# Kernel tuning notes

Measured on AMD Instinct MI355X. Metric: run time of the kernel, lower is better.

## Reference

```python
import jax, jax.numpy as jnp
import numpy as np

GROUPS = 32
EPS = 1e-5


def setup_inputs() -> dict:
    key = jax.random.key(0)
    k1, k2, k3, k4, k5 = jax.random.split(key, 5)
    B, C, H, W = 16, 256, 80, 80
    cg = C // GROUPS  # 8 channels per group
    x = jax.random.normal(k1, (B, C, H, W), dtype=jnp.float32)
    # conv1x1: Conv2d(cg, cg, 1) -> weight [cg, cg], bias [cg]
    fan_in = cg
    bound = 1.0 / np.sqrt(fan_in)
    conv_w = jax.random.uniform(k2, (cg, cg), minval=-bound, maxval=bound, dtype=jnp.float32)
    conv_b = jax.random.uniform(k3, (cg,), minval=-bound, maxval=bound, dtype=jnp.float32)
    # GroupNorm(num_groups=cg, num_channels=cg) affine params (init: ones/zeros)
    gn_w = jnp.ones((cg,), dtype=jnp.float32)
    gn_b = jnp.zeros((cg,), dtype=jnp.float32)
    return {"x": x, "conv_w": conv_w, "conv_b": conv_b, "gn_w": gn_w, "gn_b": gn_b}


def reference(x, conv_w, conv_b, gn_w, gn_b):
    b, c, h, w = x.shape
    cg = c // GROUPS
    gx = x.reshape(b * GROUPS, cg, h, w)  # [bg, cg, h, w]

    def norm(t):
        # GroupNorm with num_groups == num_channels: per-channel norm over (h, w)
        mu = jnp.mean(t, axis=(2, 3), keepdims=True)
        var = jnp.var(t, axis=(2, 3), keepdims=True)
        tn = (t - mu) * jax.lax.rsqrt(var + EPS)
        return tn * gn_w[None, :, None, None] + gn_b[None, :, None, None]

    def gate_branch(ph, pw):
        # ph: [bg, cg, h] (pooled over w), pw: [bg, cg, w] (pooled over h)
        cat = jnp.concatenate([ph, pw], axis=2)  # [bg, cg, h+w]
        hw = jnp.einsum('bcl,oc->bol', cat, conv_w) + conv_b[None, :, None]
        gh, gw = hw[:, :, :h], hw[:, :, h:]
        gated = gx * jax.nn.sigmoid(gh)[..., None] * jax.nn.sigmoid(gw)[:, :, None, :]
        return norm(gated)

    # avg-pool branch
    x1 = gate_branch(jnp.mean(gx, axis=3), jnp.mean(gx, axis=2))
    # max-pool branch
    y1 = gate_branch(jnp.max(gx, axis=3), jnp.max(gx, axis=2))

    x11 = x1.reshape(b * GROUPS, cg, h * w)
    y11 = y1.reshape(b * GROUPS, cg, h * w)
    # channel-attention vectors: softmax over the cg channel axis
    x12 = jax.nn.softmax(jnp.mean(x1, axis=(2, 3)), axis=-1)  # [bg, cg]  (avg pool)
    y12 = jax.nn.softmax(jnp.max(y1, axis=(2, 3)), axis=-1)   # [bg, cg]  (max pool)

    weights = jnp.einsum('bc,bcl->bl', x12, y11) + jnp.einsum('bc,bcl->bl', y12, x11)
    weights = weights.reshape(b * GROUPS, 1, h, w)
    return (gx * jax.nn.sigmoid(weights)).reshape(b, c, h, w)
```

## Files before the change

kernel.cpp:

```cpp
#include <hip/hip_runtime.h>
#include <math.h>

constexpr int CG   = 8;
constexpr int Hh   = 80;
constexpr int Ww   = 80;
constexpr int HW   = Hh * Ww;
constexpr int NG   = 16 * 32;
constexpr int NCH  = NG * CG;
constexpr int PP   = NCH * Hh;
constexpr float EPSf = 1e-5f;

constexpr int STATS = 4 * PP;

__device__ __forceinline__ float sigmoidf(float v) {
    return 1.0f / (1.0f + __expf(-v));
}

__global__ __launch_bounds__(256) void k_pool(const float* __restrict__ x,
                                              float* __restrict__ ws) {
    const int bgc = blockIdx.x;
    const float* base = x + (size_t)bgc * HW;
    __shared__ float tile[Hh * 84];

    for (int v = threadIdx.x; v < 1600; v += 256) {
        int h  = v / 20;
        int w0 = (v % 20) * 4;
        float4 d = ((const float4*)base)[v];
        *(float4*)&tile[h * 84 + w0] = d;
    }
    __syncthreads();

    const int t = threadIdx.x;
    if (t < 80) {
        float s = 0.f, m = -INFINITY;
        const float4* r = (const float4*)&tile[t * 84];
        #pragma unroll
        for (int i = 0; i < 20; i++) {
            float4 d = r[i];
            s += d.x + d.y + d.z + d.w;
            m = fmaxf(m, fmaxf(fmaxf(d.x, d.y), fmaxf(d.z, d.w)));
        }
        ws[0 * PP + bgc * 80 + t] = s * (1.f / 80.f);
        ws[2 * PP + bgc * 80 + t] = m;
    } else if (t >= 128 && t < 208) {
        const int c = t - 128;
        float s2 = 0.f, m2 = -INFINITY;
        #pragma unroll 8
        for (int i = 0; i < 80; i++) {
            float v = tile[i * 84 + c];
            s2 += v;
            m2 = fmaxf(m2, v);
        }
        ws[1 * PP + bgc * 80 + c] = s2 * (1.f / 80.f);
        ws[3 * PP + bgc * 80 + c] = m2;
    }
}

__global__ __launch_bounds__(256) void k_stats(const float* __restrict__ x,
                                               const float* __restrict__ conv_w,
                                               const float* __restrict__ conv_b,
                                               float* __restrict__ ws) {
    const int bgc = blockIdx.x;
    const int bg = bgc >> 3, o = bgc & 7;
    __shared__ float wsm[64];
    __shared__ float cbs[8];
    __shared__ float g[4 * 80];
    if (threadIdx.x < 64) wsm[threadIdx.x] = conv_w[threadIdx.x];
    if (threadIdx.x < 8)  cbs[threadIdx.x] = conv_b[threadIdx.x];
    __syncthreads();

    for (int i = threadIdx.x; i < 320; i += 256) {
        const int a = i / 80, p = i % 80;
        const float* pool = ws + a * PP + bg * 640;
        float acc = cbs[o];
        #pragma unroll
        for (int c = 0; c < 8; c++) acc += wsm[o * 8 + c] * pool[c * 80 + p];
        g[i] = sigmoidf(acc);
    }
    __syncthreads();

    const float* base = x + (size_t)bgc * HW;
    float s1x = 0.f, s2x = 0.f, s1y = 0.f, s2y = 0.f;
    float my = -INFINITY, ny = INFINITY;

    for (int i = 0; i < 7; i++) {
        const int v = threadIdx.x + i * 256;
        if (v < 1600) {
            const int h  = v / 20;
            const int w0 = (v % 20) * 4;
            float4 d = ((const float4*)base)[v];
            const float ghx = g[h], ghy = g[160 + h];
            float dd[4] = {d.x, d.y, d.z, d.w};
            #pragma unroll
            for (int j = 0; j < 4; j++) {
                const float tx = dd[j] * ghx * g[80 + w0 + j];
                const float ty = dd[j] * ghy * g[240 + w0 + j];
                s1x += tx; s2x += tx * tx;
                s1y += ty; s2y += ty * ty;
                my = fmaxf(my, ty); ny = fminf(ny, ty);
            }
        }
    }
    #pragma unroll
    for (int off = 32; off > 0; off >>= 1) {
        s1x += __shfl_down(s1x, off);
        s2x += __shfl_down(s2x, off);
        s1y += __shfl_down(s1y, off);
        s2y += __shfl_down(s2y, off);
        my = fmaxf(my, __shfl_down(my, off));
        ny = fminf(ny, __shfl_down(ny, off));
    }
    __shared__ float red[4][6];
    const int wave = threadIdx.x >> 6, lane = threadIdx.x & 63;
    if (lane == 0) {
        red[wave][0] = s1x; red[wave][1] = s2x; red[wave][2] = s1y;
        red[wave][3] = s2y; red[wave][4] = my;  red[wave][5] = ny;
    }
    __syncthreads();
    if (threadIdx.x == 0) {
        float a0 = red[0][0], a1 = red[0][1], a2 = red[0][2], a3 = red[0][3];
        float a4 = red[0][4], a5 = red[0][5];
        for (int wv = 1; wv < 4; wv++) {
            a0 += red[wv][0]; a1 += red[wv][1]; a2 += red[wv][2]; a3 += red[wv][3];
            a4 = fmaxf(a4, red[wv][4]); a5 = fminf(a5, red[wv][5]);
        }
        float* st = ws + STATS + bgc * 8;
        st[0] = a0; st[1] = a1; st[2] = a2; st[3] = a3; st[4] = a4; st[5] = a5;
    }
}

__global__ __launch_bounds__(256) void k_out(const float* __restrict__ x,
                                             const float* __restrict__ conv_w,
                                             const float* __restrict__ conv_b,
                                             const float* __restrict__ gnw,
                                             const float* __restrict__ gnb,
                                             const float* __restrict__ ws,
                                             float* __restrict__ out) {
    const int bg = blockIdx.x;
    __shared__ float wsm[64];
    __shared__ float cbs[8];
    __shared__ float g[4 * 640];
    __shared__ float Axs[8], Bxs[8], Ays[8], Bys[8], ymaxs[8];
    __shared__ float cHx[8], cHy[8];
    __shared__ float kcs;
    if (threadIdx.x < 64) wsm[threadIdx.x] = conv_w[threadIdx.x];
    if (threadIdx.x < 8)  cbs[threadIdx.x] = conv_b[threadIdx.x];
    __syncthreads();

    for (int i = threadIdx.x; i < 2560; i += 256) {
        const int a = i / 640, c = (i % 640) / 80, p = i % 80;
        const float* pool = ws + a * PP + bg * 640;
        float acc = cbs[c];
        #pragma unroll
        for (int cc = 0; cc < 8; cc++) acc += wsm[c * 8 + cc] * pool[cc * 80 + p];
        g[i] = sigmoidf(acc);
    }
    if (threadIdx.x < 8) {
        const int t = threadIdx.x;
        const float* st = ws + STATS + (bg * 8 + t) * 8;
        const float s1x = st[0], s2x = st[1], s1y = st[2], s2y = st[3];
        const float my = st[4], ny = st[5];
        const float w = gnw[t], b = gnb[t];
        const float mux  = s1x * (1.f / 6400.f);
        const float varx = s2x * (1.f / 6400.f) - mux * mux;
        const float ax   = rsqrtf(varx + EPSf) * w;
        Axs[t] = ax; Bxs[t] = b - mux * ax;
        const float muy  = s1y * (1.f / 6400.f);
        const float vary = s2y * (1.f / 6400.f) - muy * muy;
        const float ay   = rsqrtf(vary + EPSf) * w;
        Ays[t] = ay; Bys[t] = b - muy * ay;
        ymaxs[t] = (ay >= 0.f ? my : ny) * ay + Bys[t];
    }
    __syncthreads();
    if (threadIdx.x == 0) {
        float x12[8], y12[8];
        float mb = -INFINITY;
        for (int c = 0; c < 8; c++) mb = fmaxf(mb, gnb[c]);
        float se = 0.f;
        for (int c = 0; c < 8; c++) { x12[c] = __expf(gnb[c] - mb); se += x12[c]; }
        float inv = 1.f / se;
        for (int c = 0; c < 8; c++) x12[c] *= inv;
        float m2 = -INFINITY;
        for (int c = 0; c < 8; c++) m2 = fmaxf(m2, ymaxs[c]);
        se = 0.f;
        for (int c = 0; c < 8; c++) { y12[c] = __expf(ymaxs[c] - m2); se += y12[c]; }
        inv = 1.f / se;
        float kc = 0.f;
        for (int c = 0; c < 8; c++) {
            y12[c] *= inv;
            cHx[c] = y12[c] * Axs[c];
            cHy[c] = x12[c] * Ays[c];
            kc += x12[c] * Bys[c] + y12[c] * Bxs[c];
        }
        kcs = kc;
    }
    __syncthreads();
    for (int i = threadIdx.x; i < 1280; i += 256) {
        if (i < 640) g[i]        *= cHx[i / 80];
        else         g[640 + i]  *= cHy[(i - 640) / 80];
    }
    __syncthreads();

    const float kc = kcs;
    const float* base = x + (size_t)bg * CG * HW;
    float*       ob   = out + (size_t)bg * CG * HW;

    for (int i = 0; i < 7; i++) {
        const int v = threadIdx.x + i * 256;
        if (v < 1600) {
            const int h  = v / 20;
            const int w0 = (v % 20) * 4;
            float4 gxv[8];
            #pragma unroll
            for (int c = 0; c < 8; c++)
                gxv[c] = *(const float4*)(base + c * HW + v * 4);

            float s0 = kc, s1 = kc, s2 = kc, s3 = kc;
            #pragma unroll
            for (int c = 0; c < 8; c++) {
                const float chx = g[c * 80 + h];
                const float chy = g[1280 + c * 80 + h];
                const float* cwx = &g[640  + c * 80 + w0];
                const float* cwy = &g[1920 + c * 80 + w0];
                s0 += gxv[c].x * (chy * cwy[0] + chx * cwx[0]);
                s1 += gxv[c].y * (chy * cwy[1] + chx * cwx[1]);
                s2 += gxv[c].z * (chy * cwy[2] + chx * cwx[2]);
                s3 += gxv[c].w * (chy * cwy[3] + chx * cwx[3]);
            }
            s0 = sigmoidf(s0); s1 = sigmoidf(s1); s2 = sigmoidf(s2); s3 = sigmoidf(s3);
            #pragma unroll
            for (int c = 0; c < 8; c++) {
                float4 o;
                o.x = gxv[c].x * s0; o.y = gxv[c].y * s1;
                o.z = gxv[c].z * s2; o.w = gxv[c].w * s3;
                *(float4*)(ob + c * HW + v * 4) = o;
            }
        }
    }
}

extern "C" void kernel_launch(void* const* d_in, const int* in_sizes, int n_in,
                              void* d_out, int out_size, void* d_ws, size_t ws_size,
                              hipStream_t stream) {
    const float* x      = (const float*)d_in[0];
    const float* conv_w = (const float*)d_in[1];
    const float* conv_b = (const float*)d_in[2];
    const float* gn_w   = (const float*)d_in[3];
    const float* gn_b   = (const float*)d_in[4];
    float* out = (float*)d_out;
    float* ws  = (float*)d_ws;

    k_pool <<<NCH, 256, 0, stream>>>(x, ws);
    k_stats<<<NCH, 256, 0, stream>>>(x, conv_w, conv_b, ws);
    k_out  <<<NG,  256, 0, stream>>>(x, conv_w, conv_b, gn_w, gn_b, ws, out);
}
```

Baseline: 84.40 us.

## Fuse pooling, stats, and output kernels into one per-group kernel

Replaces the three-kernel pipeline (pool, per-channel stats, output) with a single kernel where each 512-thread block handles one group's 8 channels. Pooled values and GroupNorm statistics stay in shared memory instead of going through a global workspace, and the launches are reduced to one. The group's input is still read three times, relying on cache reuse, and the grid drops to 512 blocks with several serialised phases and barriers, which can reduce latency hiding.

Result: faster. 69.80 us (-17.3%).

```diff
diff --git a/kernel.cpp b/kernel.cpp
--- a/kernel.cpp
+++ b/kernel.cpp
@@ -1,192 +1,171 @@
 #include <hip/hip_runtime.h>
 #include <math.h>
 
-constexpr int CG   = 8;
-constexpr int Hh   = 80;
-constexpr int Ww   = 80;
-constexpr int HW   = Hh * Ww;
-constexpr int NG   = 16 * 32;
-constexpr int NCH  = NG * CG;
-constexpr int PP   = NCH * Hh;
+constexpr int CG = 8;
+constexpr int HW = 6400;
+constexpr int NG = 512;
 constexpr float EPSf = 1e-5f;
-
-constexpr int STATS = 4 * PP;
 
 __device__ __forceinline__ float sigmoidf(float v) {
     return 1.0f / (1.0f + __expf(-v));
 }
 
-__global__ __launch_bounds__(256) void k_pool(const float* __restrict__ x,
-                                              float* __restrict__ ws) {
-    const int bgc = blockIdx.x;
-    const float* base = x + (size_t)bgc * HW;
-    __shared__ float tile[Hh * 84];
-
-    for (int v = threadIdx.x; v < 1600; v += 256) {
-        int h  = v / 20;
-        int w0 = (v % 20) * 4;
-        float4 d = ((const float4*)base)[v];
-        *(float4*)&tile[h * 84 + w0] = d;
-    }
-    __syncthreads();
-
-    const int t = threadIdx.x;
-    if (t < 80) {
-        float s = 0.f, m = -INFINITY;
-        const float4* r = (const float4*)&tile[t * 84];
-        #pragma unroll
-        for (int i = 0; i < 20; i++) {
-            float4 d = r[i];
-            s += d.x + d.y + d.z + d.w;
-            m = fmaxf(m, fmaxf(fmaxf(d.x, d.y), fmaxf(d.z, d.w)));
-        }
-        ws[0 * PP + bgc * 80 + t] = s * (1.f / 80.f);
-        ws[2 * PP + bgc * 80 + t] = m;
-    } else if (t >= 128 && t < 208) {
-        const int c = t - 128;
-        float s2 = 0.f, m2 = -INFINITY;
-        #pragma unroll 8
-        for (int i = 0; i < 80; i++) {
-            float v = tile[i * 84 + c];
-            s2 += v;
-            m2 = fmaxf(m2, v);
-        }
-        ws[1 * PP + bgc * 80 + c] = s2 * (1.f / 80.f);
-        ws[3 * PP + bgc * 80 + c] = m2;
-    }
-}
-
-__global__ __launch_bounds__(256) void k_stats(const float* __restrict__ x,
-                                               const float* __restrict__ conv_w,
-                                               const float* __restrict__ conv_b,
-                                               float* __restrict__ ws) {
-    const int bgc = blockIdx.x;
-    const int bg = bgc >> 3, o = bgc & 7;
+__global__ __launch_bounds__(512, 4) void k_fused(
+    const float* __restrict__ x,
+    const float* __restrict__ conv_w,
+    const float* __restrict__ conv_b,
+    const float* __restrict__ gnw,
+    const float* __restrict__ gnb,
+    float* __restrict__ out)
+{
+    const int bg  = blockIdx.x;
+    const int tid = threadIdx.x;
+
+    __shared__ float tile[80 * 84];
+    __shared__ float pools[4 * 640];
+    __shared__ float g[4 * 640];
     __shared__ float wsm[64];
     __shared__ float cbs[8];
-    __shared__ float g[4 * 80];
-    if (threadIdx.x < 64) wsm[threadIdx.x] = conv_w[threadIdx.x];
-    if (threadIdx.x < 8)  cbs[threadIdx.x] = conv_b[threadIdx.x];
-    __syncthreads();
-
-    for (int i = threadIdx.x; i < 320; i += 256) {
-        const int a = i / 80, p = i % 80;
-        const float* pool = ws + a * PP + bg * 640;
-        float acc = cbs[o];
-        #pragma unroll
-        for (int c = 0; c < 8; c++) acc += wsm[o * 8 + c] * pool[c * 80 + p];
-        g[i] = sigmoidf(acc);
-    }
-    __syncthreads();
-
-    const float* base = x + (size_t)bgc * HW;
-    float s1x = 0.f, s2x = 0.f, s1y = 0.f, s2y = 0.f;
-    float my = -INFINITY, ny = INFINITY;
-
-    for (int i = 0; i < 7; i++) {
-        const int v = threadIdx.x + i * 256;
-        if (v < 1600) {
-            const int h  = v / 20;
-            const int w0 = (v % 20) * 4;
-            float4 d = ((const float4*)base)[v];
-            const float ghx = g[h], ghy = g[160 + h];
-            float dd[4] = {d.x, d.y, d.z, d.w};
-            #pragma unroll
-            for (int j = 0; j < 4; j++) {
-                const float tx = dd[j] * ghx * g[80 + w0 + j];
-                const float ty = dd[j] * ghy * g[240 + w0 + j];
+    __shared__ float stats[8][8];
+    __shared__ float Axs[8], Bxs[8], Ays[8], Bys[8], ymaxs[8], cHx[8], cHy[8];
+    __shared__ float kcs;
+
+    if (tid < 64) wsm[tid] = conv_w[tid];
+    if (tid < 8)  cbs[tid] = conv_b[tid];
+
+    const float* base = x + (size_t)bg * CG * HW;
+
+    for (int c = 0; c < 8; ++c) {
+        __syncthreads();
+        for (int i = 0; i < 4; ++i) {
+            const int v = tid + i * 512;
+            if (v < 1600) {
+                float4 d = ((const float4*)(base + c * HW))[v];
+                const int h = v / 20, w0 = (v % 20) * 4;
+                *(float4*)&tile[h * 84 + w0] = d;
+            }
+        }
+        __syncthreads();
+        if (tid < 320) {
+            const int r = tid >> 2, q = tid & 3;
+            float s = 0.f, m = -INFINITY;
+            const float4* rp = (const float4*)&tile[r * 84];
+            #pragma unroll
+            for (int k = q * 5; k < q * 5 + 5; ++k) {
+                float4 d = rp[k];
+                s += d.x + d.y + d.z + d.w;
+                m = fmaxf(m, fmaxf(fmaxf(d.x, d.y), fmaxf(d.z, d.w)));
+            }
+            s += __shfl_down(s, 2, 4); s += __shfl_down(s, 1, 4);
+            m = fmaxf(m, __shfl_down(m, 2, 4));
+            m = fmaxf(m, __shfl_down(m, 1, 4));
+            if (q == 0) {
+                pools[0 * 640 + c * 80 + r] = s * (1.f / 80.f);
+                pools[2 * 640 + c * 80 + r] = m;
+            }
+            float s2 = 0.f, m2 = -INFINITY;
+            #pragma unroll 4
+            for (int hh = q * 20; hh < q * 20 + 20; ++hh) {
+                const float vv = tile[hh * 84 + r];
+                s2 += vv;
+                m2 = fmaxf(m2, vv);
+            }
+            s2 += __shfl_down(s2, 2, 4); s2 += __shfl_down(s2, 1, 4);
+            m2 = fmaxf(m2, __shfl_down(m2, 2, 4));
+            m2 = fmaxf(m2, __shfl_down(m2, 1, 4));
+            if (q == 0) {
+                pools[1 * 640 + c * 80 + r] = s2 * (1.f / 80.f);
+                pools[3 * 640 + c * 80 + r] = m2;
+            }
+        }
+    }
+    __syncthreads();
+
+    for (int i = 0; i < 5; ++i) {
+        const int e = tid + i * 512;
+        if (e < 2560) {
+            const int a = e / 640, rem = e % 640, c = rem / 80, p = rem % 80;
+            float acc = cbs[c];
+            #pragma unroll
+            for (int cc = 0; cc < 8; ++cc)
+                acc += wsm[c * 8 + cc] * pools[a * 640 + cc * 80 + p];
+            g[e] = sigmoidf(acc);
+        }
+    }
+    __syncthreads();
+
+    {
+        const int c = tid >> 6, lane = tid & 63;
+        const float* cb_ = base + c * HW;
+        float s1x = 0.f, s2x = 0.f, s1y = 0.f, s2y = 0.f;
+        float my = -INFINITY, ny = INFINITY;
+        for (int j = 0; j < 25; ++j) {
+            const int v = lane + j * 64;
+            float4 d = ((const float4*)cb_)[v];
+            const int h = v / 20, w0 = (v % 20) * 4;
+            const float ghx = g[0 * 640 + c * 80 + h];
+            const float ghy = g[2 * 640 + c * 80 + h];
+            const float4 gwx = *(const float4*)&g[1 * 640 + c * 80 + w0];
+            const float4 gwy = *(const float4*)&g[3 * 640 + c * 80 + w0];
+            const float dd[4]  = {d.x, d.y, d.z, d.w};
+            const float gx4[4] = {gwx.x, gwx.y, gwx.z, gwx.w};
+            const float gy4[4] = {gwy.x, gwy.y, gwy.z, gwy.w};
+            #pragma unroll
+            for (int k = 0; k < 4; ++k) {
+                const float tx = dd[k] * ghx * gx4[k];
+                const float ty = dd[k] * ghy * gy4[k];
                 s1x += tx; s2x += tx * tx;
                 s1y += ty; s2y += ty * ty;
                 my = fmaxf(my, ty); ny = fminf(ny, ty);
             }
         }
-    }
-    #pragma unroll
-    for (int off = 32; off > 0; off >>= 1) {
-        s1x += __shfl_down(s1x, off);
-        s2x += __shfl_down(s2x, off);
-        s1y += __shfl_down(s1y, off);
-        s2y += __shfl_down(s2y, off);
-        my = fmaxf(my, __shfl_down(my, off));
-        ny = fminf(ny, __shfl_down(ny, off));
-    }
-    __shared__ float red[4][6];
-    const int wave = threadIdx.x >> 6, lane = threadIdx.x & 63;
-    if (lane == 0) {
-        red[wave][0] = s1x; red[wave][1] = s2x; red[wave][2] = s1y;
-        red[wave][3] = s2y; red[wave][4] = my;  red[wave][5] = ny;
-    }
-    __syncthreads();
-    if (threadIdx.x == 0) {
-        float a0 = red[0][0], a1 = red[0][1], a2 = red[0][2], a3 = red[0][3];
-        float a4 = red[0][4], a5 = red[0][5];
-        for (int wv = 1; wv < 4; wv++) {
-            a0 += red[wv][0]; a1 += red[wv][1]; a2 += red[wv][2]; a3 += red[wv][3];
-            a4 = fmaxf(a4, red[wv][4]); a5 = fminf(a5, red[wv][5]);
-        }
-        float* st = ws + STATS + bgc * 8;
-        st[0] = a0; st[1] = a1; st[2] = a2; st[3] = a3; st[4] = a4; st[5] = a5;
-    }
-}
-
-__global__ __launch_bounds__(256) void k_out(const float* __restrict__ x,
-                                             const float* __restrict__ conv_w,
-                                             const float* __restrict__ conv_b,
-                                             const float* __restrict__ gnw,
-                                             const float* __restrict__ gnb,
-                                             const float* __restrict__ ws,
-                                             float* __restrict__ out) {
-    const int bg = blockIdx.x;
-    __shared__ float wsm[64];
-    __shared__ float cbs[8];
-    __shared__ float g[4 * 640];
-    __shared__ float Axs[8], Bxs[8], Ays[8], Bys[8], ymaxs[8];
-    __shared__ float cHx[8], cHy[8];
-    __shared__ float kcs;
-    if (threadIdx.x < 64) wsm[threadIdx.x] = conv_w[threadIdx.x];
-    if (threadIdx.x < 8)  cbs[threadIdx.x] = conv_b[threadIdx.x];
-    __syncthreads();
-
-    for (int i = threadIdx.x; i < 2560; i += 256) {
-        const int a = i / 640, c = (i % 640) / 80, p = i % 80;
-        const float* pool = ws + a * PP + bg * 640;
-        float acc = cbs[c];
         #pragma unroll
-        for (int cc = 0; cc < 8; cc++) acc += wsm[c * 8 + cc] * pool[cc * 80 + p];
-        g[i] = sigmoidf(acc);
-    }
-    if (threadIdx.x < 8) {
-        const int t = threadIdx.x;
-        const float* st = ws + STATS + (bg * 8 + t) * 8;
-        const float s1x = st[0], s2x = st[1], s1y = st[2], s2y = st[3];
-        const float my = st[4], ny = st[5];
-        const float w = gnw[t], b = gnb[t];
+        for (int off = 32; off > 0; off >>= 1) {
+            s1x += __shfl_down(s1x, off);
+            s2x += __shfl_down(s2x, off);
+            s1y += __shfl_down(s1y, off);
+            s2y += __shfl_down(s2y, off);
+            my = fmaxf(my, __shfl_down(my, off));
+            ny = fminf(ny, __shfl_down(ny, off));
+        }
+        if (lane == 0) {
+            stats[c][0] = s1x; stats[c][1] = s2x; stats[c][2] = s1y;
+            stats[c][3] = s2y; stats[c][4] = my;  stats[c][5] = ny;
+        }
+    }
+    __syncthreads();
+
+    if (tid < 8) {
+        const float s1x = stats[tid][0], s2x = stats[tid][1];
+        const float s1y = stats[tid][2], s2y = stats[tid][3];
+        const float my  = stats[tid][4], ny  = stats[tid][5];
+        const float w = gnw[tid], b = gnb[tid];
         const float mux  = s1x * (1.f / 6400.f);
         const float varx = s2x * (1.f / 6400.f) - mux * mux;
         const float ax   = rsqrtf(varx + EPSf) * w;
-        Axs[t] = ax; Bxs[t] = b - mux * ax;
+        Axs[tid] = ax; Bxs[tid] = b - mux * ax;
         const float muy  = s1y * (1.f / 6400.f);
         const float vary = s2y * (1.f / 6400.f) - muy * muy;
         const float ay   = rsqrtf(vary + EPSf) * w;
-        Ays[t] = ay; Bys[t] = b - muy * ay;
-        ymaxs[t] = (ay >= 0.f ? my : ny) * ay + Bys[t];
-    }
-    __syncthreads();
-    if (threadIdx.x == 0) {
+        Ays[tid] = ay; Bys[tid] = b - muy * ay;
+        ymaxs[tid] = (ay >= 0.f ? my : ny) * ay + Bys[tid];
+    }
+    __syncthreads();
+    if (tid == 0) {
         float x12[8], y12[8];
         float mb = -INFINITY;
-        for (int c = 0; c < 8; c++) mb = fmaxf(mb, gnb[c]);
+        for (int c = 0; c < 8; ++c) mb = fmaxf(mb, gnb[c]);
         float se = 0.f;
-        for (int c = 0; c < 8; c++) { x12[c] = __expf(gnb[c] - mb); se += x12[c]; }
+        for (int c = 0; c < 8; ++c) { x12[c] = __expf(gnb[c] - mb); se += x12[c]; }
         float inv = 1.f / se;
-        for (int c = 0; c < 8; c++) x12[c] *= inv;
+        for (int c = 0; c < 8; ++c) x12[c] *= inv;
         float m2 = -INFINITY;
-        for (int c = 0; c < 8; c++) m2 = fmaxf(m2, ymaxs[c]);
+        for (int c = 0; c < 8; ++c) m2 = fmaxf(m2, ymaxs[c]);
         se = 0.f;
-        for (int c = 0; c < 8; c++) { y12[c] = __expf(ymaxs[c] - m2); se += y12[c]; }
+        for (int c = 0; c < 8; ++c) { y12[c] = __expf(ymaxs[c] - m2); se += y12[c]; }
         inv = 1.f / se;
         float kc = 0.f;
-        for (int c = 0; c < 8; c++) {
+        for (int c = 0; c < 8; ++c) {
             y12[c] *= inv;
             cHx[c] = y12[c] * Axs[c];
             cHy[c] = x12[c] * Ays[c];
@@ -195,41 +174,42 @@
         kcs = kc;
     }
     __syncthreads();
-    for (int i = threadIdx.x; i < 1280; i += 256) {
-        if (i < 640) g[i]        *= cHx[i / 80];
-        else         g[640 + i]  *= cHy[(i - 640) / 80];
+    for (int i = 0; i < 3; ++i) {
+        const int e = tid + i * 512;
+        if (e < 1280) {
+            if (e < 640) g[e]                 *= cHx[e / 80];
+            else         g[1280 + (e - 640)]  *= cHy[(e - 640) / 80];
+        }
     }
     __syncthreads();
 
     const float kc = kcs;
-    const float* base = x + (size_t)bg * CG * HW;
-    float*       ob   = out + (size_t)bg * CG * HW;
-
-    for (int i = 0; i < 7; i++) {
-        const int v = threadIdx.x + i * 256;
+    float* ob = out + (size_t)bg * CG * HW;
+    for (int i = 0; i < 4; ++i) {
+        const int v = tid + i * 512;
         if (v < 1600) {
-            const int h  = v / 20;
-            const int w0 = (v % 20) * 4;
+            const int h = v / 20, w0 = (v % 20) * 4;
             float4 gxv[8];
             #pragma unroll
-            for (int c = 0; c < 8; c++)
+            for (int c = 0; c < 8; ++c)
                 gxv[c] = *(const float4*)(base + c * HW + v * 4);
 
             float s0 = kc, s1 = kc, s2 = kc, s3 = kc;
             #pragma unroll
-            for (int c = 0; c < 8; c++) {
-                const float chx = g[c * 80 + h];
-                const float chy = g[1280 + c * 80 + h];
-                const float* cwx = &g[640  + c * 80 + w0];
-                const float* cwy = &g[1920 + c * 80 + w0];
-                s0 += gxv[c].x * (chy * cwy[0] + chx * cwx[0]);
-                s1 += gxv[c].y * (chy * cwy[1] + chx * cwx[1]);
-                s2 += gxv[c].z * (chy * cwy[2] + chx * cwx[2]);
-                s3 += gxv[c].w * (chy * cwy[3] + chx * cwx[3]);
-            }
-            s0 = sigmoidf(s0); s1 = sigmoidf(s1); s2 = sigmoidf(s2); s3 = sigmoidf(s3);
-            #pragma unroll
-            for (int c = 0; c < 8; c++) {
+            for (int c = 0; c < 8; ++c) {
+                const float chx = g[0 * 640 + c * 80 + h];
+                const float chy = g[2 * 640 + c * 80 + h];
+                const float4 cwx = *(const float4*)&g[1 * 640 + c * 80 + w0];
+                const float4 cwy = *(const float4*)&g[3 * 640 + c * 80 + w0];
+                s0 += gxv[c].x * (chy * cwy.x + chx * cwx.x);
+                s1 += gxv[c].y * (chy * cwy.y + chx * cwx.y);
+                s2 += gxv[c].z * (chy * cwy.z + chx * cwx.z);
+                s3 += gxv[c].w * (chy * cwy.w + chx * cwx.w);
+            }
+            s0 = sigmoidf(s0); s1 = sigmoidf(s1);
+            s2 = sigmoidf(s2); s3 = sigmoidf(s3);
+            #pragma unroll
+            for (int c = 0; c < 8; ++c) {
                 float4 o;
                 o.x = gxv[c].x * s0; o.y = gxv[c].y * s1;
                 o.z = gxv[c].z * s2; o.w = gxv[c].w * s3;
@@ -248,9 +228,7 @@
     const float* gn_w   = (const float*)d_in[3];
     const float* gn_b   = (const float*)d_in[4];
     float* out = (float*)d_out;
-    float* ws  = (float*)d_ws;
-
-    k_pool <<<NCH, 256, 0, stream>>>(x, ws);
-    k_stats<<<NCH, 256, 0, stream>>>(x, conv_w, conv_b, ws);
-    k_out  <<<NG,  256, 0, stream>>>(x, conv_w, conv_b, gn_w, gn_b, ws, out);
+    (void)d_ws; (void)ws_size;
+
+    k_fused<<<NG, 512, 0, stream>>>(x, conv_w, conv_b, gn_w, gn_b, out);
 }
```
